# Kernel optimization log

Measured on AMD Instinct MI355X. Metric: run time of the kernel, lower is better.

Reference implementation:

```python
import jax, jax.numpy as jnp
import numpy as np

LAMBDA_D = 250.0
POS_MARGIN = 1.0
NEG_MARGIN = 0.2
BLOCK = 8          # block_size in the original
DIST_THRESH = 7.5  # correspondence threshold in pixels
EPS = 1e-12        # F.normalize eps


def _l2_normalize(x, axis):
    # matches torch.nn.functional.normalize: x / max(||x||_2, eps)
    n = jnp.linalg.norm(x, axis=axis, keepdims=True)
    return x / jnp.maximum(n, EPS)


def setup_inputs() -> dict:
    key = jax.random.key(0)
    k1, k2, k3 = jax.random.split(key, 3)
    b, d, hc, wc = 2, 256, 60, 80  # 480x640 image, block 8
    desc = jax.random.normal(k1, (b, d, hc, wc), dtype=jnp.float32)
    wrap_desc = jax.random.normal(k2, (b, d, hc, wc), dtype=jnp.float32)
    # realistic near-identity homographies (random H would warp everything off-image)
    H = jnp.eye(3, dtype=jnp.float32)[None] + 0.02 * jax.random.normal(k3, (b, 3, 3), dtype=jnp.float32)
    return {"desc": desc, "wrap_desc": wrap_desc, "H": H}


def reference(desc, wrap_desc, H):
    b, d, hc, wc = desc.shape
    n = hc * wc

    # cell-center coordinates in (row, col) order, shape (hc, wc, 2)
    coords = jnp.stack(
        jnp.meshgrid(jnp.arange(hc), jnp.arange(wc), indexing="ij"), axis=-1
    ).astype(jnp.float32) * BLOCK + BLOCK // 2

    # homogeneous (x, y, 1) points, shape (n, 3)
    xy1 = jnp.concatenate(
        [coords[..., 1:2], coords[..., 0:1], jnp.ones((hc, wc, 1), jnp.float32)],
        axis=-1,
    ).reshape(n, 3)

    # warp by homography: (b, n, 3)
    w = jnp.einsum("bij,nj->bni", H, xy1)
    wxy = w[..., :2] / w[..., 2:3]                       # (b, n, 2) in (x, y)
    warp = jnp.stack([wxy[..., 1], wxy[..., 0]], axis=-1).reshape(b, hc, wc, 2)  # (row, col)

    # distance between warped query centers and all cell centers: (b, hc, wc, hc, wc)
    dist = jnp.linalg.norm(coords[None, None, None] - warp[:, :, :, None, None, :], axis=-1)
    S = (dist <= DIST_THRESH).astype(desc.dtype)

    # unit-normalized descriptors, channel-last
    dn = _l2_normalize(jnp.transpose(desc, (0, 2, 3, 1)), axis=-1)       # (b, hc, wc, d)
    wn = _l2_normalize(jnp.transpose(wrap_desc, (0, 2, 3, 1)), axis=-1)  # (b, hc, wc, d)

    # full correlation volume via batched GEMM (same math as broadcast-sum)
    dot = jax.nn.relu(jnp.einsum("bijd,bkld->bijkl", dn, wn))           # (b,hc,wc,hc,wc)

    # normalize over warped-cell axis (k, l), then over query-cell axis (i, j)
    dot = _l2_normalize(dot.reshape(b, hc, wc, n), axis=3).reshape(b, hc, wc, hc, wc)
    dot = _l2_normalize(dot.reshape(b, n, hc, wc), axis=1).reshape(b, hc, wc, hc, wc)

    loss = LAMBDA_D * S * jax.nn.relu(POS_MARGIN - dot) + (1.0 - S) * jax.nn.relu(dot - NEG_MARGIN)
    # sum over (i,j,k,l) per image / n^2, then sum over batch == total sum / n^2
    return jnp.sum(loss) / float(n * n)
```

## Files before the change

### kernel.cpp

```cpp
#include <hip/hip_runtime.h>

#define HC 60
#define WCC 80
#define NCELL 4800
#define NP 4864
#define NB 38
#define DCH 256
#define BATCH 2
#define QT 64

typedef _Float16 half8 __attribute__((ext_vector_type(8)));
typedef float f32x4 __attribute__((ext_vector_type(4)));

__device__ __forceinline__ void gload_lds16(const void* gp, void* lp) {
  __builtin_amdgcn_global_load_lds(
      (const __attribute__((address_space(1))) void*)gp,
      (__attribute__((address_space(3))) void*)lp, 16, 0, 0);
}

__global__ __launch_bounds__(256) void warp_kernel(const float* __restrict__ H,
                                                   float* __restrict__ wout) {
  int idx = blockIdx.x * 256 + threadIdx.x;
  if (idx >= BATCH * NP) return;
  int b = idx / NP;
  int q = idx - b * NP;
  float wr = 1e9f, wc = 1e9f;
  if (q < NCELL) {
    int i = q / WCC;
    int j = q - i * WCC;
    float x = (float)(j * 8 + 4);
    float y = (float)(i * 8 + 4);
    const float* h = H + b * 9;
    float w0 = h[0] * x + h[1] * y + h[2];
    float w1 = h[3] * x + h[4] * y + h[5];
    float w2 = h[6] * x + h[7] * y + h[8];
    wr = w1 / w2;
    wc = w0 / w2;
  }
  wout[2 * idx]     = wr;
  wout[2 * idx + 1] = wc;
}

__global__ __launch_bounds__(256) void normalize_kernel(
    const float* __restrict__ desc, const float* __restrict__ wdesc,
    _Float16* __restrict__ dnp, _Float16* __restrict__ wnp) {
  __shared__ _Float16 vt[DCH][QT + 2];
  __shared__ float pss[4][QT];
  __shared__ float invq[QT];
  const int q0 = blockIdx.x * QT;
  const int which = blockIdx.y;
  const int b = blockIdx.z;
  const float* in = which ? wdesc : desc;
  _Float16* out = which ? wnp : dnp;
  const int tx = threadIdx.x & 63;
  const int ty = threadIdx.x >> 6;
  const int q = q0 + tx;
  float ss = 0.f;
  for (int cc = 0; cc < DCH / 4; ++cc) {
    const int c = cc * 4 + ty;
    float v = (q < NCELL) ? in[((size_t)b * DCH + c) * NCELL + q] : 0.f;
    vt[c][tx] = (_Float16)v;
    ss += v * v;
  }
  pss[ty][tx] = ss;
  __syncthreads();
  if (ty == 0) {
    float tot = pss[0][tx] + pss[1][tx] + pss[2][tx] + pss[3][tx];
    invq[tx] = 1.f / fmaxf(sqrtf(tot), 1e-12f);
  }
  __syncthreads();
  for (int it = 0; it < QT; ++it) {
    out[((size_t)b * NP + q0 + it) * DCH + threadIdx.x] =
        (_Float16)((float)vt[threadIdx.x][it] * invq[it]);
  }
}

union GemmSmem {
  struct { _Float16 As[128][64]; _Float16 Bs[128][64]; } g;
  _Float16 rp[128][132];
};

template <int MODE, bool STOREU>
__global__ __launch_bounds__(256) void gemm_kernel(
    const _Float16* __restrict__ A, const _Float16* __restrict__ Bm,
    const float* __restrict__ invr, const float* __restrict__ colscale,
    const float* __restrict__ warp, float* __restrict__ sqacc,
    float* __restrict__ lossp, _Float16* __restrict__ uout) {
  __shared__ GemmSmem sm;
  const int tid = threadIdx.x;
  const int wave = tid >> 6;
  const int lane = tid & 63;
  const int batch = blockIdx.z;
  const int row0 = blockIdx.y * 128;
  const int col0 = blockIdx.x * 128;
  const _Float16* Ab = A + ((size_t)batch * NP + row0) * DCH;
  const _Float16* Bb = Bm + ((size_t)batch * NP + col0) * DCH;

  const int wq_r = wave >> 1;
  const int wq_c = wave & 1;
  const int g = lane >> 4;
  const int cL = lane & 15;

  f32x4 acc[4][4] = {};

  const int srow = lane >> 3;
  const int scol = lane & 7;
  const int sc_swz = (scol ^ srow) * 8;

  for (int ks = 0; ks < 4; ++ks) {
#pragma unroll
    for (int c = 0; c < 4; ++c) {
      const int chunk = wave * 4 + c;
      const int r = chunk * 8 + srow;
      gload_lds16(Ab + (size_t)r * DCH + ks * 64 + sc_swz,
                  (char*)(&sm.g.As[0][0]) + chunk * 1024);
      gload_lds16(Bb + (size_t)r * DCH + ks * 64 + sc_swz,
                  (char*)(&sm.g.Bs[0][0]) + chunk * 1024);
    }
    __syncthreads();
#pragma unroll
    for (int kk = 0; kk < 2; ++kk) {
      half8 af[4], bf[4];
#pragma unroll
      for (int m = 0; m < 4; ++m) {
        const int row = wq_r * 64 + m * 16 + cL;
        const int c16 = (kk * 4 + g) ^ (row & 7);
        af[m] = *reinterpret_cast<const half8*>(
            (const char*)(&sm.g.As[0][0]) + row * 128 + c16 * 16);
      }
#pragma unroll
      for (int n = 0; n < 4; ++n) {
        const int row = wq_c * 64 + n * 16 + cL;
        const int c16 = (kk * 4 + g) ^ (row & 7);
        bf[n] = *reinterpret_cast<const half8*>(
            (const char*)(&sm.g.Bs[0][0]) + row * 128 + c16 * 16);
      }
#pragma unroll
      for (int m = 0; m < 4; ++m)
#pragma unroll
        for (int n = 0; n < 4; ++n)
          acc[m][n] =
              __builtin_amdgcn_mfma_f32_16x16x32_f16(af[m], bf[n], acc[m][n], 0, 0, 0);
    }
    __syncthreads();
  }

  if (MODE == 0 || MODE == 1) {
    float cs[4];
    if (MODE == 1) {
#pragma unroll
      for (int n = 0; n < 4; ++n)
        cs[n] = colscale[(size_t)batch * NP + col0 + wq_c * 64 + n * 16 + cL];
    }
    float rs[4][4];
#pragma unroll
    for (int m = 0; m < 4; ++m)
#pragma unroll
      for (int j = 0; j < 4; ++j) rs[m][j] = 0.f;
#pragma unroll
    for (int m = 0; m < 4; ++m)
#pragma unroll
      for (int n = 0; n < 4; ++n)
#pragma unroll
        for (int j = 0; j < 4; ++j) {
          float u = fmaxf(acc[m][n][j], 0.f);
          if (MODE == 1) u *= cs[n];
          rs[m][j] += u * u;
        }
#pragma unroll
    for (int m = 0; m < 4; ++m)
#pragma unroll
      for (int j = 0; j < 4; ++j) {
        float v = rs[m][j];
        v += __shfl_xor(v, 1, 64);
        v += __shfl_xor(v, 2, 64);
        v += __shfl_xor(v, 4, 64);
        v += __shfl_xor(v, 8, 64);
        if (cL == 0)
          atomicAdd(&sqacc[(size_t)batch * NP + row0 + wq_r * 64 + m * 16 + g * 4 + j], v);
      }
    if (STOREU) {
#pragma unroll
      for (int m = 0; m < 4; ++m)
#pragma unroll
        for (int n = 0; n < 4; ++n)
#pragma unroll
          for (int j = 0; j < 4; ++j)
            sm.rp[wq_r * 64 + m * 16 + g * 4 + j][wq_c * 64 + n * 16 + cL] =
                (_Float16)fmaxf(acc[m][n][j], 0.f);
      __syncthreads();
      const int rl = tid >> 4;
      const int uu = tid & 15;
#pragma unroll
      for (int p = 0; p < 8; ++p) {
        const int row = p * 16 + rl;
        half8 hv = *reinterpret_cast<const half8*>(&sm.rp[row][uu * 8]);
        *reinterpret_cast<half8*>(
            &uout[((size_t)batch * NP + row0 + row) * NP + col0 + uu * 8]) = hv;
      }
    }
  } else if (MODE == 2) {
    float cy[4], cx[4], ic[4];
    int cvalid[4];
#pragma unroll
    for (int n = 0; n < 4; ++n) {
      int ct = col0 + wq_c * 64 + n * 16 + cL;
      cvalid[n] = (ct < NCELL);
      int tk = ct / WCC;
      int tl = ct - tk * WCC;
      cy[n] = (float)(tk * 8 + 4);
      cx[n] = (float)(tl * 8 + 4);
      ic[n] = colscale[(size_t)batch * NP + ct];
    }
    float lsum = 0.f;
#pragma unroll
    for (int m = 0; m < 4; ++m)
#pragma unroll
      for (int j = 0; j < 4; ++j) {
        const int rq = row0 + wq_r * 64 + m * 16 + g * 4 + j;
        if (rq < NCELL) {
          const float ir = invr[(size_t)batch * NP + rq];
          const float wr = warp[((size_t)batch * NP + rq) * 2];
          const float wcol = warp[((size_t)batch * NP + rq) * 2 + 1];
#pragma unroll
          for (int n = 0; n < 4; ++n) {
            if (cvalid[n]) {
              float u = fmaxf(acc[m][n][j], 0.f);
              float v = u * ir * ic[n];
              float dr = cy[n] - wr;
              float dc = cx[n] - wcol;
              float pos = 250.f * fmaxf(1.f - v, 0.f);
              float neg = fmaxf(v - 0.2f, 0.f);
              lsum += (dr * dr + dc * dc <= 56.25f) ? pos : neg;
            }
          }
        }
      }
#pragma unroll
    for (int s = 1; s < 64; s <<= 1) lsum += __shfl_xor(lsum, s, 64);
    if (lane == 0) {
      int slot = (((batch * NB + blockIdx.y) * NB + blockIdx.x) << 2) | wave;
      lossp[slot] = lsum;
    }
  }
}

__global__ __launch_bounds__(256) void passB_kernel(const _Float16* __restrict__ u,
                                                    const float* __restrict__ invr,
                                                    float* __restrict__ c2) {
  const int b = blockIdx.z;
  const int t0 = blockIdx.x * 2048 + threadIdx.x * 8;
  if (t0 >= NP) return;
  const int q0 = blockIdx.y * 64;
  const _Float16* up = u + ((size_t)b * NP + q0) * NP + t0;
  const float* irp = invr + b * NP + q0;
  float s[8];
#pragma unroll
  for (int i = 0; i < 8; ++i) s[i] = 0.f;
  for (int q = 0; q < 64; ++q) {
    const float ir = irp[q];
    half8 h = *reinterpret_cast<const half8*>(up);
#pragma unroll
    for (int i = 0; i < 8; ++i) {
      float v = (float)h[i] * ir;
      s[i] += v * v;
    }
    up += NP;
  }
#pragma unroll
  for (int i = 0; i < 8; ++i) atomicAdd(&c2[b * NP + t0 + i], s[i]);
}

__global__ __launch_bounds__(256) void passC_kernel(const _Float16* __restrict__ u,
                                                    const float* __restrict__ invr,
                                                    const float* __restrict__ invc,
                                                    const float* __restrict__ warp,
                                                    float* __restrict__ lossp) {
  const int b = blockIdx.z;
  const int t0 = blockIdx.x * 2048 + threadIdx.x * 8;
  const int q0 = blockIdx.y * 128;
  float cy[8], cx[8], ic[8];
  bool val[8];
  const bool active = (t0 < NP);
#pragma unroll
  for (int i = 0; i < 8; ++i) {
    const int t = active ? (t0 + i) : 0;
    val[i] = active && (t < NCELL);
    const int tk = t / WCC;
    const int tl = t - tk * WCC;
    cy[i] = (float)(tk * 8 + 4);
    cx[i] = (float)(tl * 8 + 4);
    ic[i] = invc[b * NP + t];
  }
  float lsum = 0.f;
  if (active) {
    const _Float16* up = u + ((size_t)b * NP + q0) * NP + t0;
    for (int q = 0; q < 128; ++q) {
      const int qq = q0 + q;
      const float ir = invr[b * NP + qq];
      const float wr = warp[(size_t)(b * NP + qq) * 2];
      const float wc = warp[(size_t)(b * NP + qq) * 2 + 1];
      half8 h = *reinterpret_cast<const half8*>(up);
#pragma unroll
      for (int i = 0; i < 8; ++i) {
        if (val[i]) {
          float v = (float)h[i] * ir * ic[i];
          float dr = cy[i] - wr;
          float dc = cx[i] - wc;
          float pos = 250.f * fmaxf(1.f - v, 0.f);
          float neg = fmaxf(v - 0.2f, 0.f);
          lsum += (dr * dr + dc * dc <= 56.25f) ? pos : neg;
        }
      }
      up += NP;
    }
  }
#pragma unroll
  for (int s = 1; s < 64; s <<= 1) lsum += __shfl_xor(lsum, s, 64);
  if ((threadIdx.x & 63) == 0) {
    int slot = ((((b * 38 + blockIdx.y) * 3 + blockIdx.x) << 2) | (threadIdx.x >> 6));
    lossp[slot] = lsum;
  }
}

__global__ void finalize_inv(const float* __restrict__ sq, float* __restrict__ inv,
                             int count) {
  int i = blockIdx.x * 256 + threadIdx.x;
  if (i < count) inv[i] = 1.f / fmaxf(sqrtf(sq[i]), 1e-12f);
}

__global__ __launch_bounds__(1024) void loss_reduce(const float* __restrict__ lossp,
                                                    float* __restrict__ out, int count) {
  double s = 0.0;
  for (int i = threadIdx.x; i < count; i += 1024) s += (double)lossp[i];
#pragma unroll
  for (int k = 1; k < 64; k <<= 1) s += __shfl_xor(s, k, 64);
  __shared__ double sd[16];
  if ((threadIdx.x & 63) == 0) sd[threadIdx.x >> 6] = s;
  __syncthreads();
  if (threadIdx.x == 0) {
    double t = 0.0;
    for (int w = 0; w < 16; ++w) t += sd[w];
    out[0] = (float)(t / ((double)NCELL * (double)NCELL));
  }
}

extern "C" void kernel_launch(void* const* d_in, const int* in_sizes, int n_in,
                              void* d_out, int out_size, void* d_ws, size_t ws_size,
                              hipStream_t stream) {
  const float* desc  = (const float*)d_in[0];
  const float* wdesc = (const float*)d_in[1];
  const float* H     = (const float*)d_in[2];
  char* ws = (char*)d_ws;

  constexpr size_t SZ_HALF = (size_t)BATCH * NP * DCH * sizeof(_Float16);
  constexpr size_t SZ_WARP = (size_t)BATCH * NP * 2 * sizeof(float);
  constexpr size_t SZ_VEC  = (size_t)BATCH * NP * sizeof(float);
  constexpr size_t SZ_LOSS = (size_t)BATCH * NB * NB * 4 * sizeof(float);
  constexpr size_t SZ_U    = (size_t)BATCH * NP * NP * sizeof(_Float16);
  constexpr size_t OFF_DNP  = 0;
  constexpr size_t OFF_WNP  = OFF_DNP + SZ_HALF;
  constexpr size_t OFF_WARP = OFF_WNP + SZ_HALF;
  constexpr size_t OFF_R2   = OFF_WARP + SZ_WARP;
  constexpr size_t OFF_INVR = OFF_R2 + SZ_VEC;
  constexpr size_t OFF_C2   = OFF_INVR + SZ_VEC;
  constexpr size_t OFF_INVC = OFF_C2 + SZ_VEC;
  constexpr size_t OFF_LOSS = OFF_INVC + SZ_VEC;
  constexpr size_t OFF_U    = OFF_LOSS + SZ_LOSS;
  constexpr size_t TOTAL    = OFF_U + SZ_U;

  _Float16* dnp = (_Float16*)(ws + OFF_DNP);
  _Float16* wnp = (_Float16*)(ws + OFF_WNP);
  float* warp = (float*)(ws + OFF_WARP);
  float* r2   = (float*)(ws + OFF_R2);
  float* invr = (float*)(ws + OFF_INVR);
  float* c2   = (float*)(ws + OFF_C2);
  float* invc = (float*)(ws + OFF_INVC);
  float* lossp = (float*)(ws + OFF_LOSS);
  _Float16* u = (_Float16*)(ws + OFF_U);

  hipMemsetAsync(r2, 0, 4 * SZ_VEC, stream);

  warp_kernel<<<dim3((BATCH * NP + 255) / 256), 256, 0, stream>>>(H, warp);
  normalize_kernel<<<dim3(NP / QT, 2, BATCH), 256, 0, stream>>>(desc, wdesc, dnp, wnp);

  dim3 gg(NB, NB, BATCH);
  if (ws_size >= TOTAL) {
    gemm_kernel<0, true><<<gg, 256, 0, stream>>>(dnp, wnp, nullptr, nullptr, nullptr,
                                                 r2, nullptr, u);
    finalize_inv<<<(BATCH * NP + 255) / 256, 256, 0, stream>>>(r2, invr, BATCH * NP);
    passB_kernel<<<dim3(3, 76, BATCH), 256, 0, stream>>>(u, invr, c2);
    finalize_inv<<<(BATCH * NP + 255) / 256, 256, 0, stream>>>(c2, invc, BATCH * NP);
    passC_kernel<<<dim3(3, 38, BATCH), 256, 0, stream>>>(u, invr, invc, warp, lossp);
    loss_reduce<<<1, 1024, 0, stream>>>(lossp, (float*)d_out, BATCH * 38 * 3 * 4);
  } else {
    gemm_kernel<0, false><<<gg, 256, 0, stream>>>(dnp, wnp, nullptr, nullptr, nullptr,
                                                  r2, nullptr, nullptr);
    finalize_inv<<<(BATCH * NP + 255) / 256, 256, 0, stream>>>(r2, invr, BATCH * NP);
    gemm_kernel<1, false><<<gg, 256, 0, stream>>>(wnp, dnp, nullptr, invr, nullptr,
                                                  c2, nullptr, nullptr);
    finalize_inv<<<(BATCH * NP + 255) / 256, 256, 0, stream>>>(c2, invc, BATCH * NP);
    gemm_kernel<2, false><<<gg, 256, 0, stream>>>(dnp, wnp, invr, invc, warp,
                                                  nullptr, lossp, nullptr);
    loss_reduce<<<1, 1024, 0, stream>>>(lossp, (float*)d_out, BATCH * NB * NB * 4);
  }
}
```

Before: 298.5 us.

## Retile passB/passC for more blocks and fold inverse-norm kernels inline

New measurement: 241.3 us. 19.1% less time.

```diff
diff --git a/kernel.cpp b/kernel.cpp
--- a/kernel.cpp
+++ b/kernel.cpp
@@ -246,61 +246,76 @@
 }
 
 __global__ __launch_bounds__(256) void passB_kernel(const _Float16* __restrict__ u,
-                                                    const float* __restrict__ invr,
+                                                    const float* __restrict__ r2,
                                                     float* __restrict__ c2) {
   const int b = blockIdx.z;
-  const int t0 = blockIdx.x * 2048 + threadIdx.x * 8;
-  if (t0 >= NP) return;
-  const int q0 = blockIdx.y * 64;
-  const _Float16* up = u + ((size_t)b * NP + q0) * NP + t0;
-  const float* irp = invr + b * NP + q0;
+  const int lt = threadIdx.x & 63;
+  const int lq = threadIdx.x >> 6;
+  const int t0 = blockIdx.x * 512 + lt * 8;
+  const int q0 = blockIdx.y * 64 + lq * 16;
   float s[8];
 #pragma unroll
   for (int i = 0; i < 8; ++i) s[i] = 0.f;
-  for (int q = 0; q < 64; ++q) {
-    const float ir = irp[q];
-    half8 h = *reinterpret_cast<const half8*>(up);
+  if (t0 < NP) {
+    const _Float16* up = u + ((size_t)b * NP + q0) * NP + t0;
+    const float* r2p = r2 + b * NP + q0;
+#pragma unroll 4
+    for (int q = 0; q < 16; ++q) {
+      const float ir = 1.f / fmaxf(sqrtf(r2p[q]), 1e-12f);
+      half8 h = *reinterpret_cast<const half8*>(up + (size_t)q * NP);
+#pragma unroll
+      for (int i = 0; i < 8; ++i) {
+        float v = (float)h[i] * ir;
+        s[i] += v * v;
+      }
+    }
+  }
+  __shared__ float red[4][64][9];
+#pragma unroll
+  for (int i = 0; i < 8; ++i) red[lq][lt][i] = s[i];
+  __syncthreads();
+  if (lq == 0 && t0 < NP) {
 #pragma unroll
     for (int i = 0; i < 8; ++i) {
-      float v = (float)h[i] * ir;
-      s[i] += v * v;
-    }
-    up += NP;
-  }
-#pragma unroll
-  for (int i = 0; i < 8; ++i) atomicAdd(&c2[b * NP + t0 + i], s[i]);
+      float tot = red[0][lt][i] + red[1][lt][i] + red[2][lt][i] + red[3][lt][i];
+      atomicAdd(&c2[b * NP + t0 + i], tot);
+    }
+  }
 }
 
 __global__ __launch_bounds__(256) void passC_kernel(const _Float16* __restrict__ u,
-                                                    const float* __restrict__ invr,
-                                                    const float* __restrict__ invc,
+                                                    const float* __restrict__ r2,
+                                                    const float* __restrict__ c2,
                                                     const float* __restrict__ warp,
                                                     float* __restrict__ lossp) {
   const int b = blockIdx.z;
-  const int t0 = blockIdx.x * 2048 + threadIdx.x * 8;
-  const int q0 = blockIdx.y * 128;
+  const int lt = threadIdx.x & 63;
+  const int lq = threadIdx.x >> 6;
+  const int t0 = blockIdx.x * 512 + lt * 8;
+  const int q0 = blockIdx.y * 128 + lq * 32;
   float cy[8], cx[8], ic[8];
   bool val[8];
-  const bool active = (t0 < NP);
+  const bool act = (t0 < NP);
 #pragma unroll
   for (int i = 0; i < 8; ++i) {
-    const int t = active ? (t0 + i) : 0;
-    val[i] = active && (t < NCELL);
+    const int t = act ? (t0 + i) : 0;
+    val[i] = act && (t < NCELL);
     const int tk = t / WCC;
     const int tl = t - tk * WCC;
     cy[i] = (float)(tk * 8 + 4);
     cx[i] = (float)(tl * 8 + 4);
-    ic[i] = invc[b * NP + t];
+    ic[i] = val[i] ? 1.f / fmaxf(sqrtf(c2[b * NP + t]), 1e-12f) : 0.f;
   }
   float lsum = 0.f;
-  if (active) {
+  if (act) {
     const _Float16* up = u + ((size_t)b * NP + q0) * NP + t0;
-    for (int q = 0; q < 128; ++q) {
+#pragma unroll 4
+    for (int q = 0; q < 32; ++q) {
       const int qq = q0 + q;
-      const float ir = invr[b * NP + qq];
+      const float ir = 1.f / fmaxf(sqrtf(r2[b * NP + qq]), 1e-12f);
       const float wr = warp[(size_t)(b * NP + qq) * 2];
       const float wc = warp[(size_t)(b * NP + qq) * 2 + 1];
-      half8 h = *reinterpret_cast<const half8*>(up);
+      half8 h = *reinterpret_cast<const half8*>(up + (size_t)q * NP);
 #pragma unroll
       for (int i = 0; i < 8; ++i) {
         if (val[i]) {
@@ -312,15 +327,12 @@
           lsum += (dr * dr + dc * dc <= 56.25f) ? pos : neg;
         }
       }
-      up += NP;
     }
   }
 #pragma unroll
   for (int s = 1; s < 64; s <<= 1) lsum += __shfl_xor(lsum, s, 64);
-  if ((threadIdx.x & 63) == 0) {
-    int slot = ((((b * 38 + blockIdx.y) * 3 + blockIdx.x) << 2) | (threadIdx.x >> 6));
-    lossp[slot] = lsum;
-  }
+  if (lt == 0)
+    lossp[(((b * NB + blockIdx.y) * 10 + blockIdx.x) << 2) | lq] = lsum;
 }
 
 __global__ void finalize_inv(const float* __restrict__ sq, float* __restrict__ inv,
@@ -356,30 +368,31 @@
   constexpr size_t SZ_HALF = (size_t)BATCH * NP * DCH * sizeof(_Float16);
   constexpr size_t SZ_WARP = (size_t)BATCH * NP * 2 * sizeof(float);
   constexpr size_t SZ_VEC  = (size_t)BATCH * NP * sizeof(float);
-  constexpr size_t SZ_LOSS = (size_t)BATCH * NB * NB * 4 * sizeof(float);
+  constexpr size_t SZ_LOSS = (size_t)BATCH * NB * 10 * 4 * sizeof(float);
   constexpr size_t SZ_U    = (size_t)BATCH * NP * NP * sizeof(_Float16);
   constexpr size_t OFF_DNP  = 0;
   constexpr size_t OFF_WNP  = OFF_DNP + SZ_HALF;
   constexpr size_t OFF_WARP = OFF_WNP + SZ_HALF;
   constexpr size_t OFF_R2   = OFF_WARP + SZ_WARP;
-  constexpr size_t OFF_INVR = OFF_R2 + SZ_VEC;
-  constexpr size_t OFF_C2   = OFF_INVR + SZ_VEC;
-  constexpr size_t OFF_INVC = OFF_C2 + SZ_VEC;
+  constexpr size_t OFF_C2   = OFF_R2 + SZ_VEC;
+  constexpr size_t OFF_INVR = OFF_C2 + SZ_VEC;
+  constexpr size_t OFF_INVC = OFF_INVR + SZ_VEC;
   constexpr size_t OFF_LOSS = OFF_INVC + SZ_VEC;
-  constexpr size_t OFF_U    = OFF_LOSS + SZ_LOSS;
+  constexpr size_t SZ_LOSS2 = (size_t)BATCH * NB * NB * 4 * sizeof(float);
+  constexpr size_t OFF_U    = OFF_LOSS + (SZ_LOSS > SZ_LOSS2 ? SZ_LOSS : SZ_LOSS2);
   constexpr size_t TOTAL    = OFF_U + SZ_U;
 
   _Float16* dnp = (_Float16*)(ws + OFF_DNP);
   _Float16* wnp = (_Float16*)(ws + OFF_WNP);
   float* warp = (float*)(ws + OFF_WARP);
   float* r2   = (float*)(ws + OFF_R2);
+  float* c2   = (float*)(ws + OFF_C2);
   float* invr = (float*)(ws + OFF_INVR);
-  float* c2   = (float*)(ws + OFF_C2);
   float* invc = (float*)(ws + OFF_INVC);
   float* lossp = (float*)(ws + OFF_LOSS);
   _Float16* u = (_Float16*)(ws + OFF_U);
 
-  hipMemsetAsync(r2, 0, 4 * SZ_VEC, stream);
+  hipMemsetAsync(r2, 0, 2 * SZ_VEC, stream);
 
   warp_kernel<<<dim3((BATCH * NP + 255) / 256), 256, 0, stream>>>(H, warp);
   normalize_kernel<<<dim3(NP / QT, 2, BATCH), 256, 0, stream>>>(desc, wdesc, dnp, wnp);
@@ -388,11 +401,9 @@
   if (ws_size >= TOTAL) {
     gemm_kernel<0, true><<<gg, 256, 0, stream>>>(dnp, wnp, nullptr, nullptr, nullptr,
                                                  r2, nullptr, u);
-    finalize_inv<<<(BATCH * NP + 255) / 256, 256, 0, stream>>>(r2, invr, BATCH * NP);
-    passB_kernel<<<dim3(3, 76, BATCH), 256, 0, stream>>>(u, invr, c2);
-    finalize_inv<<<(BATCH * NP + 255) / 256, 256, 0, stream>>>(c2, invc, BATCH * NP);
-    passC_kernel<<<dim3(3, 38, BATCH), 256, 0, stream>>>(u, invr, invc, warp, lossp);
-    loss_reduce<<<1, 1024, 0, stream>>>(lossp, (float*)d_out, BATCH * 38 * 3 * 4);
+    passB_kernel<<<dim3(10, 76, BATCH), 256, 0, stream>>>(u, r2, c2);
+    passC_kernel<<<dim3(10, NB, BATCH), 256, 0, stream>>>(u, r2, c2, warp, lossp);
+    loss_reduce<<<1, 1024, 0, stream>>>(lossp, (float*)d_out, BATCH * NB * 10 * 4);
   } else {
     gemm_kernel<0, false><<<gg, 256, 0, stream>>>(dnp, wnp, nullptr, nullptr, nullptr,
                                                   r2, nullptr, nullptr);
```
